# Kernel optimization log

Measured on AMD Instinct MI355X. Metric: run time of the kernel, lower is better.

The kernel has to match this reference:

```python
import jax, jax.numpy as jnp
import numpy as np

B, V, D = 128, 1024, 512

def setup_inputs() -> dict:
    key = jax.random.key(0)
    ks = jax.random.split(key, 6)
    return {
        "features": jax.random.normal(ks[0], (B, D), dtype=jnp.float32),
        "phoneme_counts": jax.random.uniform(ks[1], (V,), minval=0.01, maxval=1.0, dtype=jnp.float32),
        "total_count": jnp.asarray(float(V), dtype=jnp.float32),
        "meg_prototypes": jax.random.normal(ks[2], (V, D), dtype=jnp.float32),
        "zipf_s": jnp.asarray(1.0, dtype=jnp.float32),
        "temperature": jnp.asarray(1.0, dtype=jnp.float32),
        "W1": jax.random.normal(ks[3], (D, 2 * D), dtype=jnp.float32) * 0.02,
        "b1": jnp.zeros((D,), dtype=jnp.float32),
        "W2": jax.random.normal(ks[4], (1, D), dtype=jnp.float32) * 0.02,
        "b2": jnp.zeros((1,), dtype=jnp.float32),
    }

def _l2norm(x, axis=-1, eps=1e-12):
    n = jnp.sqrt(jnp.sum(x * x, axis=axis, keepdims=True))
    return x / jnp.maximum(n, eps)

def reference(features, phoneme_counts, total_count, meg_prototypes,
              zipf_s, temperature, W1, b1, W2, b2):
    vocab = phoneme_counts.shape[0]
    d = features.shape[1]
    # Zipf weights: rank phonemes by frequency (descending), weight = rank^{-s}
    freqs = phoneme_counts / jnp.maximum(total_count, 1.0)
    order = jnp.argsort(-freqs)  # indices sorted by descending frequency
    ranks = jnp.zeros_like(freqs).at[order].set(
        jnp.arange(1, vocab + 1, dtype=freqs.dtype))
    zw = jnp.power(jnp.maximum(ranks, 1.0), -zipf_s)
    zipf_priors = zw / jnp.maximum(zw.sum(), 1e-8)  # [V]
    # Cosine similarity / temperature
    sim = _l2norm(features) @ _l2norm(meg_prototypes).T  # [B, V]
    sim = sim / jnp.maximum(temperature, 1e-4)
    # MLP attention: split Linear(2D,D) into feature and prototype halves,
    # avoiding the materialized [B,V,2D] concat.
    Wf, Wp = W1[:, :d], W1[:, d:]  # each [D, D]
    feat_part = features @ Wf.T          # [B, D]
    proto_part = meg_prototypes @ Wp.T   # [V, D]
    h = jax.nn.relu(feat_part[:, None, :] + proto_part[None, :, :] + b1)  # [B, V, D]
    attn = jax.nn.sigmoid(jnp.einsum('bvd,d->bv', h, W2[0]) + b2[0])      # [B, V]
    weights = zipf_priors[None, :] * (1.0 + sim) * attn
    return jax.nn.softmax(weights, axis=-1)
```

## Files before the change

### kernel.cpp

```cpp
#include <hip/hip_runtime.h>
#include <hip/hip_bf16.h>


typedef __attribute__((ext_vector_type(8))) short bhalf8;
typedef __attribute__((ext_vector_type(4))) float f32x4;

static __device__ __forceinline__ unsigned short f2bf(float x) {
    union { __hip_bfloat16 h; unsigned short u; } cv;
    cv.h = __float2bfloat16(x);
    return cv.u;
}

static __device__ __forceinline__ int4 pack_bf16_8(float4 x, float4 y) {
    union { ushort u[8]; int4 v; } r;
    r.u[0] = f2bf(x.x); r.u[1] = f2bf(x.y); r.u[2] = f2bf(x.z); r.u[3] = f2bf(x.w);
    r.u[4] = f2bf(y.x); r.u[5] = f2bf(y.y); r.u[6] = f2bf(y.z); r.u[7] = f2bf(y.w);
    return r.v;
}

__global__ __launch_bounds__(256) void gemm_prep_kernel(
    const float* __restrict__ feat, const float* __restrict__ counts,
    const float* __restrict__ proto, const float* __restrict__ zs,
    const float* __restrict__ W1, const float* __restrict__ b1,
    float* __restrict__ fpT, unsigned short* __restrict__ ppbT,
    float* __restrict__ dotraw,
    float* __restrict__ zw, float* __restrict__ invf, float* __restrict__ invp)
{
    int bx = blockIdx.x, tid = threadIdx.x;

    if (bx >= 176) {
        if (bx < 192) {
            __shared__ float cn[1024];
            ((float4*)cn)[tid] = ((const float4*)counts)[tid];
            __syncthreads();
            int il = tid >> 2, q = tid & 3;
            int i = (bx - 176) * 64 + il;
            float ci = cn[i];
            int cnt = 0;
            int j0 = q * 256;
            for (int j = j0; j < j0 + 256; ++j) {
                float cj = cn[j];
                cnt += (cj > ci) ? 1 : 0;
                cnt += (cj == ci && j < i) ? 1 : 0;
            }
            cnt += __shfl_xor(cnt, 1);
            cnt += __shfl_xor(cnt, 2);
            if (q == 0) zw[i] = powf((float)(cnt + 1), -zs[0]);
        } else {
            int nb = bx - 192;
            int w = tid >> 6, lane = tid & 63;
            int row = nb * 4 + w;
            const float* src = (row < 128) ? (feat + (size_t)row * 512)
                                           : (proto + (size_t)(row - 128) * 512);
            const float4* rp = (const float4*)src;
            float4 a = rp[lane * 2], b = rp[lane * 2 + 1];
            float ss = a.x*a.x + a.y*a.y + a.z*a.z + a.w*a.w
                     + b.x*b.x + b.y*b.y + b.z*b.z + b.w*b.w;
            for (int o = 32; o; o >>= 1) ss += __shfl_xor(ss, o);
            if (lane == 0) {
                float inv = 1.0f / fmaxf(sqrtf(ss), 1e-12f);
                if (row < 128) invf[row] = inv; else invp[row - 128] = inv;
            }
        }
        return;
    }

    const float* A; const float* Bm;
    int lda, ldb, tm, tn, mode;
    if (bx < 16) {
        A = feat; lda = 512; Bm = W1; ldb = 1024; mode = 0;
        tm = bx >> 3; tn = bx & 7;
    } else if (bx < 144) {
        int t = bx - 16;
        A = W1 + 512; lda = 1024; Bm = proto; ldb = 512; mode = 1;
        tm = t >> 4; tn = t & 15;
    } else {
        int t = bx - 144;
        A = feat; lda = 512; Bm = proto; ldb = 512; mode = 2;
        tm = t >> 4; tn = t & 15;
    }

    __shared__ unsigned short As[64 * 40];
    __shared__ unsigned short Bs[64 * 40];

    int r = tid >> 2, kq = (tid & 3) * 8;
    int wave = tid >> 6, lane = tid & 63;
    int fr = lane & 15, quad = lane >> 4;

    const float* Ag = A + (size_t)(tm * 64 + r) * lda + kq;
    const float* Bg = Bm + (size_t)(tn * 64 + r) * ldb + kq;

    float4 a0 = *(const float4*)(Ag),     a1 = *(const float4*)(Ag + 4);
    float4 g0 = *(const float4*)(Bg),     g1 = *(const float4*)(Bg + 4);

    f32x4 acc0 = {0.f, 0.f, 0.f, 0.f};
    f32x4 acc1 = acc0, acc2 = acc0, acc3 = acc0;

    for (int kc = 0; kc < 512; kc += 32) {
        __syncthreads();
        *(int4*)&As[r * 40 + kq] = pack_bf16_8(a0, a1);
        *(int4*)&Bs[r * 40 + kq] = pack_bf16_8(g0, g1);
        __syncthreads();
        if (kc + 32 < 512) {
            a0 = *(const float4*)(Ag + kc + 32); a1 = *(const float4*)(Ag + kc + 36);
            g0 = *(const float4*)(Bg + kc + 32); g1 = *(const float4*)(Bg + kc + 36);
        }
        bhalf8 af  = *(const bhalf8*)&As[(wave * 16 + fr) * 40 + quad * 8];
        bhalf8 bf0 = *(const bhalf8*)&Bs[(fr) * 40 + quad * 8];
        bhalf8 bf1 = *(const bhalf8*)&Bs[(16 + fr) * 40 + quad * 8];
        bhalf8 bf2 = *(const bhalf8*)&Bs[(32 + fr) * 40 + quad * 8];
        bhalf8 bf3 = *(const bhalf8*)&Bs[(48 + fr) * 40 + quad * 8];
        acc0 = __builtin_amdgcn_mfma_f32_16x16x32_bf16(af, bf0, acc0, 0, 0, 0);
        acc1 = __builtin_amdgcn_mfma_f32_16x16x32_bf16(af, bf1, acc1, 0, 0, 0);
        acc2 = __builtin_amdgcn_mfma_f32_16x16x32_bf16(af, bf2, acc2, 0, 0, 0);
        acc3 = __builtin_amdgcn_mfma_f32_16x16x32_bf16(af, bf3, acc3, 0, 0, 0);
    }

    int m0 = tm * 64 + wave * 16 + quad * 4;
    int n0 = tn * 64 + fr;
    f32x4 accs[4] = {acc0, acc1, acc2, acc3};
    if (mode == 0) {
        for (int j = 0; j < 4; ++j)
            for (int rr = 0; rr < 4; ++rr)
                fpT[(size_t)(n0 + j * 16) * 128 + m0 + rr] = accs[j][rr];
    } else if (mode == 1) {
        float bv4[4];
        for (int rr = 0; rr < 4; ++rr) bv4[rr] = b1[m0 + rr];
        for (int j = 0; j < 4; ++j)
            for (int rr = 0; rr < 4; ++rr)
                ppbT[(size_t)(m0 + rr) * 1024 + n0 + j * 16] = f2bf(accs[j][rr] + bv4[rr]);
    } else {
        for (int j = 0; j < 4; ++j)
            for (int rr = 0; rr < 4; ++rr)
                dotraw[(size_t)(m0 + rr) * 1024 + n0 + j * 16] = accs[j][rr];
    }
}

__global__ __launch_bounds__(256) void hs_kernel(
    const float* __restrict__ fpT, const unsigned short* __restrict__ ppbT,
    const float* __restrict__ W2, float* __restrict__ hsp)
{
    int bx = blockIdx.x, tid = threadIdx.x;
    int bg = bx & 15, vh = (bx >> 4) & 1, ks = bx >> 5;
    int b0 = bg * 8, v = vh * 512 + tid * 2, k0 = ks * 32;

    float acc[8][2] = {};
    #pragma unroll 8
    for (int kk = 0; kk < 32; ++kk) {
        int k = k0 + kk;
        unsigned int u = *(const unsigned int*)(ppbT + (size_t)k * 1024 + v);
        float px = __uint_as_float(u << 16);
        float py = __uint_as_float(u & 0xffff0000u);
        float w2k = W2[k];
        float4 fa = *(const float4*)(fpT + (size_t)k * 128 + b0);
        float4 fb = *(const float4*)(fpT + (size_t)k * 128 + b0 + 4);
        float f[8] = {fa.x, fa.y, fa.z, fa.w, fb.x, fb.y, fb.z, fb.w};
        #pragma unroll
        for (int i = 0; i < 8; ++i) {
            acc[i][0] += fmaxf(f[i] + px, 0.f) * w2k;
            acc[i][1] += fmaxf(f[i] + py, 0.f) * w2k;
        }
    }
    float* o = hsp + ((size_t)ks * 128 + b0) * 1024 + v;
    #pragma unroll
    for (int i = 0; i < 8; ++i)
        *(float2*)(o + (size_t)i * 1024) = make_float2(acc[i][0], acc[i][1]);
}

__global__ __launch_bounds__(256) void combine_kernel(
    const float* __restrict__ dotraw, const float* __restrict__ hsp,
    const float* __restrict__ zw,
    const float* __restrict__ invf, const float* __restrict__ invp,
    const float* __restrict__ temp, const float* __restrict__ b2,
    float* __restrict__ out)
{
    int b = blockIdx.x, tid = threadIdx.x;
    int wave = tid >> 6, lane = tid & 63;
    int v = tid * 4;
    __shared__ float red[4];

    float it  = invf[b] / fmaxf(temp[0], 1e-4f);
    float b2v = b2[0];

    float4 zw4 = *(const float4*)(zw + v);
    float4 dr  = *(const float4*)(dotraw + (size_t)b * 1024 + v);
    float4 ip4 = *(const float4*)(invp + v);

    float4 h = {0.f, 0.f, 0.f, 0.f};
    #pragma unroll
    for (int s = 0; s < 16; ++s) {
        float4 hp = *(const float4*)(hsp + ((size_t)s * 128 + b) * 1024 + v);
        h.x += hp.x; h.y += hp.y; h.z += hp.z; h.w += hp.w;
    }

    float zs4 = zw4.x + zw4.y + zw4.z + zw4.w;
    for (int o = 32; o; o >>= 1) zs4 += __shfl_xor(zs4, o);
    if (lane == 0) red[wave] = zs4;
    __syncthreads();
    float izw = 1.0f / fmaxf(red[0] + red[1] + red[2] + red[3], 1e-8f);
    __syncthreads();

    float4 w;
    {
        float s0 = dr.x * it * ip4.x, s1 = dr.y * it * ip4.y;
        float s2 = dr.z * it * ip4.z, s3 = dr.w * it * ip4.w;
        float g0 = h.x + b2v, g1 = h.y + b2v, g2 = h.z + b2v, g3 = h.w + b2v;
        w.x = (zw4.x * izw) * (1.0f + s0) * (1.0f / (1.0f + expf(-g0)));
        w.y = (zw4.y * izw) * (1.0f + s1) * (1.0f / (1.0f + expf(-g1)));
        w.z = (zw4.z * izw) * (1.0f + s2) * (1.0f / (1.0f + expf(-g2)));
        w.w = (zw4.w * izw) * (1.0f + s3) * (1.0f / (1.0f + expf(-g3)));
    }

    float mx = fmaxf(fmaxf(w.x, w.y), fmaxf(w.z, w.w));
    for (int o = 32; o; o >>= 1) mx = fmaxf(mx, __shfl_xor(mx, o));
    if (lane == 0) red[wave] = mx;
    __syncthreads();
    mx = fmaxf(fmaxf(red[0], red[1]), fmaxf(red[2], red[3]));
    __syncthreads();

    float4 e;
    e.x = expf(w.x - mx); e.y = expf(w.y - mx);
    e.z = expf(w.z - mx); e.w = expf(w.w - mx);
    float sm = e.x + e.y + e.z + e.w;
    for (int o = 32; o; o >>= 1) sm += __shfl_xor(sm, o);
    if (lane == 0) red[wave] = sm;
    __syncthreads();
    float inv = 1.0f / (red[0] + red[1] + red[2] + red[3]);

    float4 r4;
    r4.x = e.x * inv; r4.y = e.y * inv; r4.z = e.z * inv; r4.w = e.w * inv;
    *(float4*)(out + (size_t)b * 1024 + v) = r4;
}

extern "C" void kernel_launch(void* const* d_in, const int* in_sizes, int n_in,
                              void* d_out, int out_size, void* d_ws, size_t ws_size,
                              hipStream_t stream) {
    const float* feat   = (const float*)d_in[0];
    const float* counts = (const float*)d_in[1];
    const float* proto  = (const float*)d_in[3];
    const float* zs     = (const float*)d_in[4];
    const float* temp   = (const float*)d_in[5];
    const float* W1     = (const float*)d_in[6];
    const float* b1     = (const float*)d_in[7];
    const float* W2     = (const float*)d_in[8];
    const float* b2     = (const float*)d_in[9];

    char* ws = (char*)d_ws;
    float* zw     = (float*)(ws + 0);
    float* invf   = (float*)(ws + 4096);
    float* invp   = (float*)(ws + 4608);
    float* fpT    = (float*)(ws + 8704);
    float* dotraw = (float*)(ws + 270848);
    unsigned short* ppbT = (unsigned short*)(ws + 795136);
    float* hsp    = (float*)(ws + 1843712);

    gemm_prep_kernel<<<480, 256, 0, stream>>>(feat, counts, proto, zs, W1, b1,
                                              fpT, ppbT, dotraw, zw, invf, invp);
    hs_kernel<<<512, 256, 0, stream>>>(fpT, ppbT, W2, hsp);
    combine_kernel<<<128, 256, 0, stream>>>(dotraw, hsp, zw, invf, invp,
                                            temp, b2, (float*)d_out);
}
```

Measured before the change: 101.2 us.

## Double-buffer GEMM LDS with K=64 steps, split hs blocks finer, widen combine blocks

The GEMM loop now stages 64-wide K chunks into double-buffered shared memory, which halves the number of barriers per tile and issues two MFMA steps per stage. The hs kernel covers 4 batch rows per block instead of 8, doubling the grid to 1024 blocks for more parallelism at the cost of re-reading ppbT more often. The combine kernel uses 1024 threads per row with one element each and 16-wave reductions, in place of 256 threads handling float4s. Shared memory use grows, and the scalar loads in combine are narrower than before.

Result: no change. 100.4 us (-0.7%).

```diff
diff --git a/kernel.cpp b/kernel.cpp
--- a/kernel.cpp
+++ b/kernel.cpp
@@ -80,40 +80,52 @@
         tm = t >> 4; tn = t & 15;
     }
 
-    __shared__ unsigned short As[64 * 40];
-    __shared__ unsigned short Bs[64 * 40];
-
-    int r = tid >> 2, kq = (tid & 3) * 8;
+    __shared__ unsigned short As[2][64 * 72];
+    __shared__ unsigned short Bs[2][64 * 72];
+
+    int r = tid >> 2, kq = (tid & 3) * 16;
     int wave = tid >> 6, lane = tid & 63;
     int fr = lane & 15, quad = lane >> 4;
 
     const float* Ag = A + (size_t)(tm * 64 + r) * lda + kq;
     const float* Bg = Bm + (size_t)(tn * 64 + r) * ldb + kq;
 
-    float4 a0 = *(const float4*)(Ag),     a1 = *(const float4*)(Ag + 4);
-    float4 g0 = *(const float4*)(Bg),     g1 = *(const float4*)(Bg + 4);
+    float4 a0 = *(const float4*)(Ag),      a1 = *(const float4*)(Ag + 4);
+    float4 a2 = *(const float4*)(Ag + 8),  a3 = *(const float4*)(Ag + 12);
+    float4 g0 = *(const float4*)(Bg),      g1 = *(const float4*)(Bg + 4);
+    float4 g2 = *(const float4*)(Bg + 8),  g3 = *(const float4*)(Bg + 12);
 
     f32x4 acc0 = {0.f, 0.f, 0.f, 0.f};
     f32x4 acc1 = acc0, acc2 = acc0, acc3 = acc0;
 
-    for (int kc = 0; kc < 512; kc += 32) {
+    for (int kc = 0; kc < 512; kc += 64) {
+        int p = (kc >> 6) & 1;
+        *(int4*)&As[p][r * 72 + kq]     = pack_bf16_8(a0, a1);
+        *(int4*)&As[p][r * 72 + kq + 8] = pack_bf16_8(a2, a3);
+        *(int4*)&Bs[p][r * 72 + kq]     = pack_bf16_8(g0, g1);
+        *(int4*)&Bs[p][r * 72 + kq + 8] = pack_bf16_8(g2, g3);
         __syncthreads();
-        *(int4*)&As[r * 40 + kq] = pack_bf16_8(a0, a1);
-        *(int4*)&Bs[r * 40 + kq] = pack_bf16_8(g0, g1);
-        __syncthreads();
-        if (kc + 32 < 512) {
-            a0 = *(const float4*)(Ag + kc + 32); a1 = *(const float4*)(Ag + kc + 36);
-            g0 = *(const float4*)(Bg + kc + 32); g1 = *(const float4*)(Bg + kc + 36);
-        }
-        bhalf8 af  = *(const bhalf8*)&As[(wave * 16 + fr) * 40 + quad * 8];
-        bhalf8 bf0 = *(const bhalf8*)&Bs[(fr) * 40 + quad * 8];
-        bhalf8 bf1 = *(const bhalf8*)&Bs[(16 + fr) * 40 + quad * 8];
-        bhalf8 bf2 = *(const bhalf8*)&Bs[(32 + fr) * 40 + quad * 8];
-        bhalf8 bf3 = *(const bhalf8*)&Bs[(48 + fr) * 40 + quad * 8];
-        acc0 = __builtin_amdgcn_mfma_f32_16x16x32_bf16(af, bf0, acc0, 0, 0, 0);
-        acc1 = __builtin_amdgcn_mfma_f32_16x16x32_bf16(af, bf1, acc1, 0, 0, 0);
-        acc2 = __builtin_amdgcn_mfma_f32_16x16x32_bf16(af, bf2, acc2, 0, 0, 0);
-        acc3 = __builtin_amdgcn_mfma_f32_16x16x32_bf16(af, bf3, acc3, 0, 0, 0);
+        if (kc + 64 < 512) {
+            const float* An = Ag + kc + 64;
+            const float* Bn = Bg + kc + 64;
+            a0 = *(const float4*)(An);     a1 = *(const float4*)(An + 4);
+            a2 = *(const float4*)(An + 8); a3 = *(const float4*)(An + 12);
+            g0 = *(const float4*)(Bn);     g1 = *(const float4*)(Bn + 4);
+            g2 = *(const float4*)(Bn + 8); g3 = *(const float4*)(Bn + 12);
+        }
+        #pragma unroll
+        for (int s = 0; s < 2; ++s) {
+            int ko = s * 32 + quad * 8;
+            bhalf8 af  = *(const bhalf8*)&As[p][(wave * 16 + fr) * 72 + ko];
+            bhalf8 bf0 = *(const bhalf8*)&Bs[p][(fr) * 72 + ko];
+            bhalf8 bf1 = *(const bhalf8*)&Bs[p][(16 + fr) * 72 + ko];
+            bhalf8 bf2 = *(const bhalf8*)&Bs[p][(32 + fr) * 72 + ko];
+            bhalf8 bf3 = *(const bhalf8*)&Bs[p][(48 + fr) * 72 + ko];
+            acc0 = __builtin_amdgcn_mfma_f32_16x16x32_bf16(af, bf0, acc0, 0, 0, 0);
+            acc1 = __builtin_amdgcn_mfma_f32_16x16x32_bf16(af, bf1, acc1, 0, 0, 0);
+            acc2 = __builtin_amdgcn_mfma_f32_16x16x32_bf16(af, bf2, acc2, 0, 0, 0);
+            acc3 = __builtin_amdgcn_mfma_f32_16x16x32_bf16(af, bf3, acc3, 0, 0, 0);
+        }
     }
 
     int m0 = tm * 64 + wave * 16 + quad * 4;
@@ -141,10 +153,10 @@
     const float* __restrict__ W2, float* __restrict__ hsp)
 {
     int bx = blockIdx.x, tid = threadIdx.x;
-    int bg = bx & 15, vh = (bx >> 4) & 1, ks = bx >> 5;
-    int b0 = bg * 8, v = vh * 512 + tid * 2, k0 = ks * 32;
-
-    float acc[8][2] = {};
+    int bg = bx & 31, vh = (bx >> 5) & 1, ks = bx >> 6;
+    int b0 = bg * 4, v = vh * 512 + tid * 2, k0 = ks * 32;
+
+    float acc[4][2] = {};
     #pragma unroll 8
     for (int kk = 0; kk < 32; ++kk) {
         int k = k0 + kk;
@@ -153,21 +165,20 @@
         float py = __uint_as_float(u & 0xffff0000u);
         float w2k = W2[k];
         float4 fa = *(const float4*)(fpT + (size_t)k * 128 + b0);
-        float4 fb = *(const float4*)(fpT + (size_t)k * 128 + b0 + 4);
-        float f[8] = {fa.x, fa.y, fa.z, fa.w, fb.x, fb.y, fb.z, fb.w};
+        float f[4] = {fa.x, fa.y, fa.z, fa.w};
         #pragma unroll
-        for (int i = 0; i < 8; ++i) {
+        for (int i = 0; i < 4; ++i) {
             acc[i][0] += fmaxf(f[i] + px, 0.f) * w2k;
             acc[i][1] += fmaxf(f[i] + py, 0.f) * w2k;
         }
     }
     float* o = hsp + ((size_t)ks * 128 + b0) * 1024 + v;
     #pragma unroll
-    for (int i = 0; i < 8; ++i)
+    for (int i = 0; i < 4; ++i)
         *(float2*)(o + (size_t)i * 1024) = make_float2(acc[i][0], acc[i][1]);
 }
 
-__global__ __launch_bounds__(256) void combine_kernel(
+__global__ __launch_bounds__(1024) void combine_kernel(
     const float* __restrict__ dotraw, const float* __restrict__ hsp,
     const float* __restrict__ zw,
     const float* __restrict__ invf, const float* __restrict__ invp,
@@ -176,60 +187,54 @@
 {
     int b = blockIdx.x, tid = threadIdx.x;
     int wave = tid >> 6, lane = tid & 63;
-    int v = tid * 4;
-    __shared__ float red[4];
+    int v = tid;
+    __shared__ float red[16];
 
     float it  = invf[b] / fmaxf(temp[0], 1e-4f);
     float b2v = b2[0];
 
-    float4 zw4 = *(const float4*)(zw + v);
-    float4 dr  = *(const float4*)(dotraw + (size_t)b * 1024 + v);
-    float4 ip4 = *(const float4*)(invp + v);
-
-    float4 h = {0.f, 0.f, 0.f, 0.f};
-    #pragma unroll
-    for (int s = 0; s < 16; ++s) {
-        float4 hp = *(const float4*)(hsp + ((size_t)s * 128 + b) * 1024 + v);
-        h.x += hp.x; h.y += hp.y; h.z += hp.z; h.w += hp.w;
-    }
-
-    float zs4 = zw4.x + zw4.y + zw4.z + zw4.w;
+    float zwv = zw[v];
+    float dr  = dotraw[(size_t)b * 1024 + v];
+    float ipv = invp[v];
+
+    float h = 0.f;
+    #pragma unroll
+    for (int s = 0; s < 16; ++s)
+        h += hsp[((size_t)s * 128 + b) * 1024 + v];
+
+    float zs4 = zwv;
     for (int o = 32; o; o >>= 1) zs4 += __shfl_xor(zs4, o);
     if (lane == 0) red[wave] = zs4;
     __syncthreads();
-    float izw = 1.0f / fmaxf(red[0] + red[1] + red[2] + red[3], 1e-8f);
-    __syncthreads();
-
-    float4 w;
-    {
-        float s0 = dr.x * it * ip4.x, s1 = dr.y * it * ip4.y;
-        float s2 = dr.z * it * ip4.z, s3 = dr.w * it * ip4.w;
-        float g0 = h.x + b2v, g1 = h.y + b2v, g2 = h.z + b2v, g3 = h.w + b2v;
-        w.x = (zw4.x * izw) * (1.0f + s0) * (1.0f / (1.0f + expf(-g0)));
-        w.y = (zw4.y * izw) * (1.0f + s1) * (1.0f / (1.0f + expf(-g1)));
-        w.z = (zw4.z * izw) * (1.0f + s2) * (1.0f / (1.0f + expf(-g2)));
-        w.w = (zw4.w * izw) * (1.0f + s3) * (1.0f / (1.0f + expf(-g3)));
-    }
-
-    float mx = fmaxf(fmaxf(w.x, w.y), fmaxf(w.z, w.w));
+    float zsum = 0.f;
+    #pragma unroll
+    for (int i = 0; i < 16; ++i) zsum += red[i];
+    float izw = 1.0f / fmaxf(zsum, 1e-8f);
+    __syncthreads();
+
+    float sim = dr * it * ipv;
+    float g = h + b2v;
+    float w = (zwv * izw) * (1.0f + sim) * (1.0f / (1.0f + expf(-g)));
+
+    float mx = w;
     for (int o = 32; o; o >>= 1) mx = fmaxf(mx, __shfl_xor(mx, o));
     if (lane == 0) red[wave] = mx;
     __syncthreads();
-    mx = fmaxf(fmaxf(red[0], red[1]), fmaxf(red[2], red[3]));
-    __syncthreads();
-
-    float4 e;
-    e.x = expf(w.x - mx); e.y = expf(w.y - mx);
-    e.z = expf(w.z - mx); e.w = expf(w.w - mx);
-    float sm = e.x + e.y + e.z + e.w;
+    mx = red[0];
+    #pragma unroll
+    for (int i = 1; i < 16; ++i) mx = fmaxf(mx, red[i]);
+    __syncthreads();
+
+    float e = expf(w - mx);
+    float sm = e;
     for (int o = 32; o; o >>= 1) sm += __shfl_xor(sm, o);
     if (lane == 0) red[wave] = sm;
     __syncthreads();
-    float inv = 1.0f / (red[0] + red[1] + red[2] + red[3]);
-
-    float4 r4;
-    r4.x = e.x * inv; r4.y = e.y * inv; r4.z = e.z * inv; r4.w = e.w * inv;
-    *(float4*)(out + (size_t)b * 1024 + v) = r4;
+    float tot = 0.f;
+    #pragma unroll
+    for (int i = 0; i < 16; ++i) tot += red[i];
+
+    out[(size_t)b * 1024 + v] = e / tot;
 }
 
 extern "C" void kernel_launch(void* const* d_in, const int* in_sizes, int n_in,
@@ -256,7 +261,7 @@
 
     gemm_prep_kernel<<<480, 256, 0, stream>>>(feat, counts, proto, zs, W1, b1,
                                               fpT, ppbT, dotraw, zw, invf, invp);
-    hs_kernel<<<512, 256, 0, stream>>>(fpT, ppbT, W2, hsp);
-    combine_kernel<<<128, 256, 0, stream>>>(dotraw, hsp, zw, invf, invp,
-                                            temp, b2, (float*)d_out);
-}
+    hs_kernel<<<1024, 256, 0, stream>>>(fpT, ppbT, W2, hsp);
+    combine_kernel<<<128, 1024, 0, stream>>>(dotraw, hsp, zw, invf, invp,
+                                             temp, b2, (float*)d_out);
+}
```
